# Performance work log

Hardware: AMD Instinct MI355X
Metric: run time of the kernel (lower is better)

The kernel has to match this reference:

```python
import jax, jax.numpy as jnp
import numpy as np

S, B, D = 2048, 2, 1024          # seq, batch, hidden
E, K = 64, 2                     # num_experts, top_k
I, SI = 512, 512                 # moe_intermediate, shared_expert_intermediate
CAP = 256                        # per-expert capacity; mean load = S*B*K/E = 128, 256 is >16 sigma -> no drops


def setup_inputs() -> dict:
    key = jax.random.key(0)
    ks = jax.random.split(key, 8)
    sc = lambda d: 1.0 / np.sqrt(d)
    return {
        "hidden_states": jax.random.normal(ks[0], (S, B, D), jnp.float32),
        "router_w": jax.random.normal(ks[1], (E, D), jnp.float32) * sc(D),          # FujiTopKRouter.weight
        "gate_up_proj": jax.random.normal(ks[2], (E, 2 * I, D), jnp.float32) * sc(D),
        "down_proj": jax.random.normal(ks[3], (E, D, I), jnp.float32) * sc(I),
        "sh_gate_w": jax.random.normal(ks[4], (SI, D), jnp.float32) * sc(D),
        "sh_up_w": jax.random.normal(ks[5], (SI, D), jnp.float32) * sc(D),
        "sh_down_w": jax.random.normal(ks[6], (D, SI), jnp.float32) * sc(SI),
        "sh_expert_gate_w": jax.random.normal(ks[7], (1, D), jnp.float32) * sc(D),
    }


def _moe(x, router_w, gate_up_proj, down_proj, sh_gate_w, sh_up_w, sh_down_w, sh_expert_gate_w):
    T = x.shape[0]
    # ---- shared expert (SwiGLU) + sigmoid gate ----
    shared = jnp.dot(jax.nn.silu(x @ sh_gate_w.T) * (x @ sh_up_w.T), sh_down_w.T)
    shared = jax.nn.sigmoid(x @ sh_expert_gate_w.T) * shared                      # [T, D]
    # ---- router: softmax (fp32) -> top-k -> normalize ----
    probs = jax.nn.softmax((x @ router_w.T).astype(jnp.float32), axis=-1)         # [T, E]
    top_w, top_i = jax.lax.top_k(probs, K)                                        # [T, K]
    top_w = top_w / (jnp.sum(top_w, axis=-1, keepdims=True) + 1e-9)
    top_w = top_w.astype(x.dtype)
    # ---- dispatch: permute (token, slot) pairs into fixed-capacity expert buffers ----
    e_f = top_i.reshape(-1)                                                       # [T*K] expert id per pair
    w_f = top_w.reshape(-1)                                                       # [T*K]
    tok = jnp.arange(T * K) // K                                                  # [T*K] source token
    oh = jax.nn.one_hot(e_f, E, dtype=jnp.int32)                                  # [T*K, E]
    pos = jnp.sum(jnp.cumsum(oh, axis=0) * oh, axis=-1) - 1                       # slot within expert
    buf = jnp.zeros((E, CAP, D), x.dtype).at[e_f, pos].set(x[tok])                # [E, C, D]
    # ---- per-expert SwiGLU as batched GEMMs ----
    h = jnp.einsum('ecd,eid->eci', buf, gate_up_proj)                             # [E, C, 2I]
    g, u = jnp.split(h, 2, axis=-1)
    y = jnp.einsum('eci,edi->ecd', jax.nn.silu(g) * u, down_proj)                 # [E, C, D]
    # ---- combine: gather back, weight, scatter-add to tokens ----
    routed = jnp.zeros_like(x).at[tok].add(y[e_f, pos] * w_f[:, None])            # [T, D]
    return shared + routed, probs


def reference(hidden_states, router_w, gate_up_proj, down_proj,
              sh_gate_w, sh_up_w, sh_down_w, sh_expert_gate_w):
    s, b, d = hidden_states.shape
    x = hidden_states.reshape(-1, d)
    out, router_logits = _moe(x, router_w, gate_up_proj, down_proj,
                              sh_gate_w, sh_up_w, sh_down_w, sh_expert_gate_w)
    return out.reshape(s, b, d), router_logits
```

## Files before the change

kernel.cpp:

```cpp
#include <hip/hip_runtime.h>
#include <hip/hip_bf16.h>
#include <stdint.h>

#define T_TOK 4096
#define DDIM  1024
#define NEXP  64
#define IDIM  512
#define SIDIM 512
#define CAP   256
#define LSTR  40

typedef __attribute__((ext_vector_type(4))) float f32x4;
typedef __attribute__((ext_vector_type(8))) short bf16x8;

__device__ __forceinline__ bf16x8 cvt8(f32x4 a, f32x4 b) {
    union { __hip_bfloat162 h[4]; bf16x8 v; } u;
    u.h[0] = __float22bfloat162_rn(make_float2(a[0], a[1]));
    u.h[1] = __float22bfloat162_rn(make_float2(a[2], a[3]));
    u.h[2] = __float22bfloat162_rn(make_float2(b[0], b[1]));
    u.h[3] = __float22bfloat162_rn(make_float2(b[2], b[3]));
    return u.v;
}
__device__ __forceinline__ short f2bs(float f) {
    union { __hip_bfloat16 h; short s; } u; u.h = __float2bfloat16(f); return u.s;
}

__global__ __launch_bounds__(256) void logits_kernel(const float* __restrict__ X,
                                                     const float* __restrict__ RW,
                                                     float* __restrict__ lpart) {
    __shared__ float sX[64 * 33];
    __shared__ float sW[64 * 33];
    int m0 = blockIdx.x * 64;
    int kz = blockIdx.y;
    int kbase = kz * 256;
    int tid = threadIdx.x;
    int tg = tid >> 4;
    int eg = tid & 15;
    float acc[4][4] = {};
    for (int k0 = 0; k0 < 256; k0 += 32) {
        __syncthreads();
#pragma unroll
        for (int i = 0; i < 8; ++i) {
            int idx = i * 256 + tid;
            int r = idx >> 5, c = idx & 31;
            sX[r * 33 + c] = X[(size_t)(m0 + r) * DDIM + kbase + k0 + c];
            sW[r * 33 + c] = RW[(size_t)r * DDIM + kbase + k0 + c];
        }
        __syncthreads();
#pragma unroll 4
        for (int k = 0; k < 32; ++k) {
            float xv[4], wv[4];
#pragma unroll
            for (int i = 0; i < 4; ++i) xv[i] = sX[(tg * 4 + i) * 33 + k];
#pragma unroll
            for (int j = 0; j < 4; ++j) wv[j] = sW[(eg * 4 + j) * 33 + k];
#pragma unroll
            for (int i = 0; i < 4; ++i)
#pragma unroll
                for (int j = 0; j < 4; ++j) acc[i][j] += xv[i] * wv[j];
        }
    }
    float* outp = lpart + (size_t)kz * T_TOK * NEXP;
#pragma unroll
    for (int i = 0; i < 4; ++i)
#pragma unroll
        for (int j = 0; j < 4; ++j)
            outp[(size_t)(m0 + tg * 4 + i) * NEXP + eg * 4 + j] = acc[i][j];
}

__global__ __launch_bounds__(256) void topk_kernel(const float* __restrict__ lpart,
                                                   const float* __restrict__ X,
                                                   const float* __restrict__ SEG,
                                                   float* __restrict__ probs_out,
                                                   int* __restrict__ counts,
                                                   int* __restrict__ tok_slot,
                                                   float* __restrict__ w_slot,
                                                   float* __restrict__ gate_sh) {
    int lane = threadIdx.x & 63;
    int wv   = threadIdx.x >> 6;
    int t    = blockIdx.x * 4 + wv;
    size_t li = (size_t)t * NEXP + lane;
    float l = lpart[li] + lpart[(size_t)T_TOK * NEXP + li]
            + lpart[2 * (size_t)T_TOK * NEXP + li] + lpart[3 * (size_t)T_TOK * NEXP + li];
    float mx = l;
    for (int s = 32; s; s >>= 1) mx = fmaxf(mx, __shfl_xor(mx, s));
    float e = __expf(l - mx);
    float sum = e;
    for (int s = 32; s; s >>= 1) sum += __shfl_xor(sum, s);
    float prob = e / sum;
    probs_out[li] = prob;
    float v = prob; int idx = lane;
    for (int s = 32; s; s >>= 1) {
        float ov = __shfl_xor(v, s); int oi = __shfl_xor(idx, s);
        if (ov > v || (ov == v && oi < idx)) { v = ov; idx = oi; }
    }
    float v1 = v; int i1 = idx;
    v = (lane == i1) ? -1e30f : prob; idx = lane;
    for (int s = 32; s; s >>= 1) {
        float ov = __shfl_xor(v, s); int oi = __shfl_xor(idx, s);
        if (ov > v || (ov == v && oi < idx)) { v = ov; idx = oi; }
    }
    float v2 = v; int i2 = idx;
    float denom = v1 + v2 + 1e-9f;
    if (lane == 0) {
        int s1 = atomicAdd(&counts[i1], 1);
        if (s1 < CAP) { tok_slot[i1 * CAP + s1] = t; w_slot[i1 * CAP + s1] = v1 / denom; }
        int s2 = atomicAdd(&counts[i2], 1);
        if (s2 < CAP) { tok_slot[i2 * CAP + s2] = t; w_slot[i2 * CAP + s2] = v2 / denom; }
    }
    float g = 0.f;
    const float* xr = X + (size_t)t * DDIM + lane * 16;
    const float* sr = SEG + lane * 16;
#pragma unroll
    for (int j = 0; j < 4; ++j) {
        f32x4 xv = *(const f32x4*)(xr + j * 4);
        f32x4 sv = *(const f32x4*)(sr + j * 4);
#pragma unroll
        for (int q = 0; q < 4; ++q) g += xv[q] * sv[q];
    }
    for (int s = 32; s; s >>= 1) g += __shfl_xor(g, s);
    if (lane == 0) gate_sh[t] = 1.f / (1.f + __expf(-g));
}

template <bool EXPERT>
__global__ __launch_bounds__(256) void gateup_kernel(const float* __restrict__ X,
                                                     const float* __restrict__ Wg_base,
                                                     const float* __restrict__ Wu_base,
                                                     const int* __restrict__ counts,
                                                     const int* __restrict__ tok_slot,
                                                     short* __restrict__ act_out) {
    __shared__ short sA[128 * LSTR];
    __shared__ short sBg[64 * LSTR];
    __shared__ short sBu[64 * LSTR];
    int e  = EXPERT ? blockIdx.z : 0;
    int m0 = blockIdx.y * 128;
    int n0 = blockIdx.x * 64;
    int M;
    const float *Wg, *Wu;
    if (EXPERT) {
        M = counts[e]; if (M > CAP) M = CAP;
        if (m0 >= M) return;
        const float* base = Wg_base + (size_t)e * (2 * IDIM) * DDIM;
        Wg = base; Wu = base + (size_t)IDIM * DDIM;
    } else {
        M = T_TOK; Wg = Wg_base; Wu = Wu_base;
    }
    int tid = threadIdx.x, lane = tid & 63, wv = tid >> 6;
    int wm = wv >> 1, wn = wv & 1;
    int srow = lane >> 2, scol8 = (lane & 3) * 8;
    const float* ag[2];
#pragma unroll
    for (int j = 0; j < 2; ++j) {
        int row = m0 + j * 64 + wv * 16 + srow;
        int grow;
        if (EXPERT) {
            int rr = (row < M) ? row : (M - 1);
            grow = tok_slot[e * CAP + rr];
        } else grow = row;
        ag[j] = X + (size_t)grow * DDIM + scol8;
    }
    const float* bgp = Wg + (size_t)(n0 + wv * 16 + srow) * DDIM + scol8;
    const float* bup = Wu + (size_t)(n0 + wv * 16 + srow) * DDIM + scol8;
    f32x4 accg[4][2] = {}; f32x4 accu[4][2] = {};
    int fm = lane & 15, fk = (lane >> 4) * 8;

    f32x4 r0[8], r1[8];
    auto loadt = [&](f32x4 (&r)[8], int k0) {
#pragma unroll
        for (int j = 0; j < 2; ++j) {
            r[j * 2 + 0] = *(const f32x4*)(ag[j] + k0);
            r[j * 2 + 1] = *(const f32x4*)(ag[j] + k0 + 4);
        }
        r[4] = *(const f32x4*)(bgp + k0); r[5] = *(const f32x4*)(bgp + k0 + 4);
        r[6] = *(const f32x4*)(bup + k0); r[7] = *(const f32x4*)(bup + k0 + 4);
    };
    auto stage = [&](const f32x4 (&r)[8]) {
        bf16x8 va0 = cvt8(r[0], r[1]);
        bf16x8 va1 = cvt8(r[2], r[3]);
        bf16x8 vg  = cvt8(r[4], r[5]);
        bf16x8 vu  = cvt8(r[6], r[7]);
        __syncthreads();
        *(bf16x8*)&sA[(wv * 16 + srow) * LSTR + scol8] = va0;
        *(bf16x8*)&sA[(64 + wv * 16 + srow) * LSTR + scol8] = va1;
        *(bf16x8*)&sBg[(wv * 16 + srow) * LSTR + scol8] = vg;
        *(bf16x8*)&sBu[(wv * 16 + srow) * LSTR + scol8] = vu;
        __syncthreads();
        bf16x8 bg[2], bu[2];
#pragma unroll
        for (int nt = 0; nt < 2; ++nt) {
            bg[nt] = *(const bf16x8*)&sBg[(wn * 32 + nt * 16 + fm) * LSTR + fk];
            bu[nt] = *(const bf16x8*)&sBu[(wn * 32 + nt * 16 + fm) * LSTR + fk];
        }
#pragma unroll
        for (int mt = 0; mt < 4; ++mt) {
            bf16x8 a = *(const bf16x8*)&sA[(wm * 64 + mt * 16 + fm) * LSTR + fk];
#pragma unroll
            for (int nt = 0; nt < 2; ++nt) {
                accg[mt][nt] = __builtin_amdgcn_mfma_f32_16x16x32_bf16(a, bg[nt], accg[mt][nt], 0, 0, 0);
                accu[mt][nt] = __builtin_amdgcn_mfma_f32_16x16x32_bf16(a, bu[nt], accu[mt][nt], 0, 0, 0);
            }
        }
    };
    loadt(r0, 0);
    for (int k0 = 0; k0 < DDIM; k0 += 64) {
        loadt(r1, k0 + 32);
        stage(r0);
        loadt(r0, (k0 + 64 < DDIM) ? (k0 + 64) : 0);
        stage(r1);
    }
    int frow = (lane >> 4) * 4, fcol = lane & 15;
    size_t out_base = EXPERT ? (size_t)e * CAP * IDIM : 0;
#pragma unroll
    for (int mt = 0; mt < 4; ++mt)
#pragma unroll
        for (int r = 0; r < 4; ++r) {
            int row = m0 + wm * 64 + mt * 16 + frow + r;
            if (row < M) {
#pragma unroll
                for (int nt = 0; nt < 2; ++nt) {
                    float g = accg[mt][nt][r];
                    float u = accu[mt][nt][r];
                    float a = (g / (1.f + __expf(-g))) * u;
                    act_out[out_base + (size_t)row * IDIM + (n0 + wn * 32 + nt * 16 + fcol)] = f2bs(a);
                }
            }
        }
}

template <bool EXPERT>
__global__ __launch_bounds__(256) void down_kernel(const short* __restrict__ A_base,
                                                   const float* __restrict__ W_base,
                                                   const int* __restrict__ counts,
                                                   const int* __restrict__ tok_slot,
                                                   const float* __restrict__ w_slot,
                                                   const float* __restrict__ gate_sh,
                                                   float* __restrict__ out) {
    __shared__ short sA[128 * LSTR];
    __shared__ short sB[128 * LSTR];
    const int KD = IDIM;
    int e  = EXPERT ? blockIdx.z : 0;
    int m0 = blockIdx.y * 128;
    int n0 = blockIdx.x * 128;
    int M;
    const short* A;
    const float* W;
    if (EXPERT) {
        M = counts[e]; if (M > CAP) M = CAP;
        if (m0 >= M) return;
        A = A_base + (size_t)e * CAP * IDIM;
        W = W_base + (size_t)e * DDIM * IDIM;
    } else { M = T_TOK; A = A_base; W = W_base; }
    int tid = threadIdx.x, lane = tid & 63, wv = tid >> 6;
    int wm = wv >> 1, wn = wv & 1;
    int srow = lane >> 2, scol8 = (lane & 3) * 8;
    const short* ap[2];
    const float* bp[2];
#pragma unroll
    for (int j = 0; j < 2; ++j) {
        int r = j * 64 + wv * 16 + srow;
        ap[j] = A + (size_t)(m0 + r) * KD + scol8;
        bp[j] = W + (size_t)(n0 + r) * KD + scol8;
    }
    f32x4 acc[4][4] = {};
    int fm = lane & 15, fk = (lane >> 4) * 8;

    struct Buf { bf16x8 a[2]; f32x4 b[4]; };
    Buf u0, u1;
    auto loadt = [&](Buf& r, int k0) {
#pragma unroll
        for (int j = 0; j < 2; ++j) {
            r.a[j] = *(const bf16x8*)(ap[j] + k0);
            r.b[j * 2 + 0] = *(const f32x4*)(bp[j] + k0);
            r.b[j * 2 + 1] = *(const f32x4*)(bp[j] + k0 + 4);
        }
    };
    auto stage = [&](const Buf& r) {
        bf16x8 vb0 = cvt8(r.b[0], r.b[1]);
        bf16x8 vb1 = cvt8(r.b[2], r.b[3]);
        __syncthreads();
        *(bf16x8*)&sA[(wv * 16 + srow) * LSTR + scol8] = r.a[0];
        *(bf16x8*)&sA[(64 + wv * 16 + srow) * LSTR + scol8] = r.a[1];
        *(bf16x8*)&sB[(wv * 16 + srow) * LSTR + scol8] = vb0;
        *(bf16x8*)&sB[(64 + wv * 16 + srow) * LSTR + scol8] = vb1;
        __syncthreads();
        bf16x8 b[4];
#pragma unroll
        for (int nt = 0; nt < 4; ++nt)
            b[nt] = *(const bf16x8*)&sB[(wn * 64 + nt * 16 + fm) * LSTR + fk];
#pragma unroll
        for (int mt = 0; mt < 4; ++mt) {
            bf16x8 a = *(const bf16x8*)&sA[(wm * 64 + mt * 16 + fm) * LSTR + fk];
#pragma unroll
            for (int nt = 0; nt < 4; ++nt)
                acc[mt][nt] = __builtin_amdgcn_mfma_f32_16x16x32_bf16(a, b[nt], acc[mt][nt], 0, 0, 0);
        }
    };
    loadt(u0, 0);
    for (int k0 = 0; k0 < KD; k0 += 64) {
        loadt(u1, k0 + 32);
        stage(u0);
        loadt(u0, (k0 + 64 < KD) ? (k0 + 64) : 0);
        stage(u1);
    }
    int frow = (lane >> 4) * 4, fcol = lane & 15;
#pragma unroll
    for (int mt = 0; mt < 4; ++mt)
#pragma unroll
        for (int r = 0; r < 4; ++r) {
            int row = m0 + wm * 64 + mt * 16 + frow + r;
            if (row >= M) continue;
            float scale; int trow;
            if (EXPERT) { scale = w_slot[e * CAP + row]; trow = tok_slot[e * CAP + row]; }
            else        { scale = gate_sh[row];          trow = row; }
#pragma unroll
            for (int nt = 0; nt < 4; ++nt) {
                int col = n0 + wn * 64 + nt * 16 + fcol;
                float vv = acc[mt][nt][r] * scale;
                if (EXPERT) atomicAdd(&out[(size_t)trow * DDIM + col], vv);
                else        out[(size_t)trow * DDIM + col] = vv;
            }
        }
}

extern "C" void kernel_launch(void* const* d_in, const int* in_sizes, int n_in,
                              void* d_out, int out_size, void* d_ws, size_t ws_size,
                              hipStream_t stream) {
    const float* X   = (const float*)d_in[0];
    const float* RW  = (const float*)d_in[1];
    const float* GUP = (const float*)d_in[2];
    const float* DW  = (const float*)d_in[3];
    const float* SG  = (const float*)d_in[4];
    const float* SU  = (const float*)d_in[5];
    const float* SD  = (const float*)d_in[6];
    const float* SEG = (const float*)d_in[7];
    float* out = (float*)d_out;

    char* ws = (char*)d_ws;
    size_t off = 0;
    float* lpart    = (float*)(ws + off); off += 4 * (size_t)T_TOK * NEXP * 4;
    int*   counts   = (int*)  (ws + off); off += 1024;
    int*   tok_slot = (int*)  (ws + off); off += (size_t)NEXP * CAP * 4;
    float* w_slot   = (float*)(ws + off); off += (size_t)NEXP * CAP * 4;
    float* gate_sh  = (float*)(ws + off); off += (size_t)T_TOK * 4;
    short* act      = (short*)(ws + off); off += (size_t)NEXP * CAP * IDIM * 2;
    short* act_sh   = (short*)(ws + off); off += (size_t)T_TOK * SIDIM * 2;
    (void)ws_size; (void)in_sizes; (void)n_in; (void)out_size;

    hipMemsetAsync(counts, 0, NEXP * sizeof(int), stream);
    logits_kernel<<<dim3(T_TOK / 64, 4), 256, 0, stream>>>(X, RW, lpart);
    topk_kernel<<<T_TOK / 4, 256, 0, stream>>>(lpart, X, SEG,
                                               out + (size_t)T_TOK * DDIM,
                                               counts, tok_slot, w_slot, gate_sh);
    gateup_kernel<false><<<dim3(SIDIM / 64, T_TOK / 128, 1), 256, 0, stream>>>(
        X, SG, SU, nullptr, nullptr, act_sh);
    gateup_kernel<true><<<dim3(IDIM / 64, CAP / 128, NEXP), 256, 0, stream>>>(
        X, GUP, GUP, counts, tok_slot, act);
    down_kernel<false><<<dim3(DDIM / 128, T_TOK / 128, 1), 256, 0, stream>>>(
        act_sh, SD, nullptr, nullptr, nullptr, gate_sh, out);
    down_kernel<true><<<dim3(DDIM / 128, CAP / 128, NEXP), 256, 0, stream>>>(
        act, DW, counts, tok_slot, w_slot, nullptr, out);
}
```

Before: 639.4 us.

## Stream GEMM tiles directly into swizzled LDS with async double buffering

The gate-up and down GEMM kernels stop staging tiles through registers with in-register bf16 conversion. They now issue global_load_lds copies of raw fp32 (and bf16 activation) tiles into XOR-swizzled, double-buffered LDS, and convert to bf16 when fragments are read. The goal is to overlap global loads with MFMA work and cut register pressure and VALU staging. In exchange, LDS use per block is larger, which is bounded by new occupancy hints, and the fp32-to-bf16 conversion is repeated by each wave that reads a fragment.

Measured after the change: 669.0 us. 4.6% more time.

```diff
diff --git a/kernel.cpp b/kernel.cpp
--- a/kernel.cpp
+++ b/kernel.cpp
@@ -8,7 +8,6 @@
 #define IDIM  512
 #define SIDIM 512
 #define CAP   256
-#define LSTR  40
 
 typedef __attribute__((ext_vector_type(4))) float f32x4;
 typedef __attribute__((ext_vector_type(8))) short bf16x8;
@@ -23,6 +22,19 @@
 }
 __device__ __forceinline__ short f2bs(float f) {
     union { __hip_bfloat16 h; short s; } u; u.h = __float2bfloat16(f); return u.s;
+}
+
+__device__ __forceinline__ void gload16(const void* g, void* l) {
+    __builtin_amdgcn_global_load_lds((const __attribute__((address_space(1))) void*)g,
+                                     (__attribute__((address_space(3))) void*)l, 16, 0, 0);
+}
+
+__device__ __forceinline__ bf16x8 frag32(const char* reg0, int row, int s) {
+    const char* p = reg0 + row * 128;
+    int sw = row & 7;
+    f32x4 lo = *(const f32x4*)(p + (((2 * s) ^ sw) << 4));
+    f32x4 hi = *(const f32x4*)(p + (((2 * s + 1) ^ sw) << 4));
+    return cvt8(lo, hi);
 }
 
 __global__ __launch_bounds__(256) void logits_kernel(const float* __restrict__ X,
@@ -123,15 +135,13 @@
 }
 
 template <bool EXPERT>
-__global__ __launch_bounds__(256) void gateup_kernel(const float* __restrict__ X,
-                                                     const float* __restrict__ Wg_base,
-                                                     const float* __restrict__ Wu_base,
-                                                     const int* __restrict__ counts,
-                                                     const int* __restrict__ tok_slot,
-                                                     short* __restrict__ act_out) {
-    __shared__ short sA[128 * LSTR];
-    __shared__ short sBg[64 * LSTR];
-    __shared__ short sBu[64 * LSTR];
+__global__ __launch_bounds__(256, 2) void gateup_kernel(const float* __restrict__ X,
+                                                        const float* __restrict__ Wg_base,
+                                                        const float* __restrict__ Wu_base,
+                                                        const int* __restrict__ counts,
+                                                        const int* __restrict__ tok_slot,
+                                                        short* __restrict__ act_out) {
+    __shared__ char smem[2 * 32768];
     int e  = EXPERT ? blockIdx.z : 0;
     int m0 = blockIdx.y * 128;
     int n0 = blockIdx.x * 64;
@@ -147,53 +157,51 @@
     }
     int tid = threadIdx.x, lane = tid & 63, wv = tid >> 6;
     int wm = wv >> 1, wn = wv & 1;
-    int srow = lane >> 2, scol8 = (lane & 3) * 8;
-    const float* ag[2];
-#pragma unroll
-    for (int j = 0; j < 2; ++j) {
-        int row = m0 + j * 64 + wv * 16 + srow;
+
+    int srow8 = tid >> 3;
+    int scol  = (tid & 7) ^ (srow8 & 7);
+    const float* gp[8];
+#pragma unroll
+    for (int t = 0; t < 4; ++t) {
+        int row = t * 32 + srow8;
         int grow;
         if (EXPERT) {
-            int rr = (row < M) ? row : (M - 1);
+            int rr = m0 + row; if (rr >= M) rr = M - 1;
             grow = tok_slot[e * CAP + rr];
-        } else grow = row;
-        ag[j] = X + (size_t)grow * DDIM + scol8;
-    }
-    const float* bgp = Wg + (size_t)(n0 + wv * 16 + srow) * DDIM + scol8;
-    const float* bup = Wu + (size_t)(n0 + wv * 16 + srow) * DDIM + scol8;
-    f32x4 accg[4][2] = {}; f32x4 accu[4][2] = {};
-    int fm = lane & 15, fk = (lane >> 4) * 8;
-
-    f32x4 r0[8], r1[8];
-    auto loadt = [&](f32x4 (&r)[8], int k0) {
-#pragma unroll
-        for (int j = 0; j < 2; ++j) {
-            r[j * 2 + 0] = *(const f32x4*)(ag[j] + k0);
-            r[j * 2 + 1] = *(const f32x4*)(ag[j] + k0 + 4);
-        }
-        r[4] = *(const f32x4*)(bgp + k0); r[5] = *(const f32x4*)(bgp + k0 + 4);
-        r[6] = *(const f32x4*)(bup + k0); r[7] = *(const f32x4*)(bup + k0 + 4);
+        } else grow = m0 + row;
+        gp[t] = X + (size_t)grow * DDIM + scol * 4;
+    }
+#pragma unroll
+    for (int t = 0; t < 2; ++t) {
+        int row = t * 32 + srow8;
+        gp[4 + t] = Wg + (size_t)(n0 + row) * DDIM + scol * 4;
+        gp[6 + t] = Wu + (size_t)(n0 + row) * DDIM + scol * 4;
+    }
+
+    auto issue = [&](int buf) {
+        char* lb = smem + buf * 32768 + wv * 1024;
+#pragma unroll
+        for (int t = 0; t < 8; ++t) {
+            gload16(gp[t], lb + t * 4096);
+            gp[t] += 32;
+        }
     };
-    auto stage = [&](const f32x4 (&r)[8]) {
-        bf16x8 va0 = cvt8(r[0], r[1]);
-        bf16x8 va1 = cvt8(r[2], r[3]);
-        bf16x8 vg  = cvt8(r[4], r[5]);
-        bf16x8 vu  = cvt8(r[6], r[7]);
-        __syncthreads();
-        *(bf16x8*)&sA[(wv * 16 + srow) * LSTR + scol8] = va0;
-        *(bf16x8*)&sA[(64 + wv * 16 + srow) * LSTR + scol8] = va1;
-        *(bf16x8*)&sBg[(wv * 16 + srow) * LSTR + scol8] = vg;
-        *(bf16x8*)&sBu[(wv * 16 + srow) * LSTR + scol8] = vu;
-        __syncthreads();
+
+    int fm = lane & 15, s = lane >> 4;
+    f32x4 accg[4][2] = {}, accu[4][2] = {};
+    auto compute = [&](int buf) {
+        const char* bb = smem + buf * 32768;
         bf16x8 bg[2], bu[2];
 #pragma unroll
         for (int nt = 0; nt < 2; ++nt) {
-            bg[nt] = *(const bf16x8*)&sBg[(wn * 32 + nt * 16 + fm) * LSTR + fk];
-            bu[nt] = *(const bf16x8*)&sBu[(wn * 32 + nt * 16 + fm) * LSTR + fk];
+            int row = wn * 32 + nt * 16 + fm;
+            bg[nt] = frag32(bb + 16384, row, s);
+            bu[nt] = frag32(bb + 24576, row, s);
         }
 #pragma unroll
         for (int mt = 0; mt < 4; ++mt) {
-            bf16x8 a = *(const bf16x8*)&sA[(wm * 64 + mt * 16 + fm) * LSTR + fk];
+            int row = wm * 64 + mt * 16 + fm;
+            bf16x8 a = frag32(bb, row, s);
 #pragma unroll
             for (int nt = 0; nt < 2; ++nt) {
                 accg[mt][nt] = __builtin_amdgcn_mfma_f32_16x16x32_bf16(a, bg[nt], accg[mt][nt], 0, 0, 0);
@@ -201,13 +209,18 @@
             }
         }
     };
-    loadt(r0, 0);
-    for (int k0 = 0; k0 < DDIM; k0 += 64) {
-        loadt(r1, k0 + 32);
-        stage(r0);
-        loadt(r0, (k0 + 64 < DDIM) ? (k0 + 64) : 0);
-        stage(r1);
-    }
+
+    issue(0);
+#pragma unroll 1
+    for (int kt = 0; kt < 32; kt += 2) {
+        __syncthreads();
+        issue(1);
+        compute(0);
+        __syncthreads();
+        if (kt + 2 < 32) issue(0);
+        compute(1);
+    }
+
     int frow = (lane >> 4) * 4, fcol = lane & 15;
     size_t out_base = EXPERT ? (size_t)e * CAP * IDIM : 0;
 #pragma unroll
@@ -228,15 +241,14 @@
 }
 
 template <bool EXPERT>
-__global__ __launch_bounds__(256) void down_kernel(const short* __restrict__ A_base,
-                                                   const float* __restrict__ W_base,
-                                                   const int* __restrict__ counts,
-                                                   const int* __restrict__ tok_slot,
-                                                   const float* __restrict__ w_slot,
-                                                   const float* __restrict__ gate_sh,
-                                                   float* __restrict__ out) {
-    __shared__ short sA[128 * LSTR];
-    __shared__ short sB[128 * LSTR];
+__global__ __launch_bounds__(256, 3) void down_kernel(const short* __restrict__ A_base,
+                                                      const float* __restrict__ W_base,
+                                                      const int* __restrict__ counts,
+                                                      const int* __restrict__ tok_slot,
+                                                      const float* __restrict__ w_slot,
+                                                      const float* __restrict__ gate_sh,
+                                                      float* __restrict__ out) {
+    __shared__ char smem[2 * 24576];
     const int KD = IDIM;
     int e  = EXPERT ? blockIdx.z : 0;
     int m0 = blockIdx.y * 128;
@@ -252,56 +264,70 @@
     } else { M = T_TOK; A = A_base; W = W_base; }
     int tid = threadIdx.x, lane = tid & 63, wv = tid >> 6;
     int wm = wv >> 1, wn = wv & 1;
-    int srow = lane >> 2, scol8 = (lane & 3) * 8;
+
     const short* ap[2];
-    const float* bp[2];
-#pragma unroll
-    for (int j = 0; j < 2; ++j) {
-        int r = j * 64 + wv * 16 + srow;
-        ap[j] = A + (size_t)(m0 + r) * KD + scol8;
-        bp[j] = W + (size_t)(n0 + r) * KD + scol8;
-    }
+#pragma unroll
+    for (int t = 0; t < 2; ++t) {
+        int row = t * 64 + (tid >> 2);
+        int col = (tid & 3) ^ ((tid >> 2) & 3);
+        ap[t] = A + (size_t)(m0 + row) * KD + col * 8;
+    }
+    const float* bp[4];
+    {
+        int srow8 = tid >> 3;
+        int col = (tid & 7) ^ (srow8 & 7);
+#pragma unroll
+        for (int t = 0; t < 4; ++t) {
+            int row = t * 32 + srow8;
+            bp[t] = W + (size_t)(n0 + row) * KD + col * 4;
+        }
+    }
+
+    auto issue = [&](int buf) {
+        char* lb = smem + buf * 24576 + wv * 1024;
+#pragma unroll
+        for (int t = 0; t < 2; ++t) {
+            gload16(ap[t], lb + t * 4096);
+            ap[t] += 32;
+        }
+#pragma unroll
+        for (int t = 0; t < 4; ++t) {
+            gload16(bp[t], lb + 8192 + t * 4096);
+            bp[t] += 32;
+        }
+    };
+
+    int fm = lane & 15, s = lane >> 4;
     f32x4 acc[4][4] = {};
-    int fm = lane & 15, fk = (lane >> 4) * 8;
-
-    struct Buf { bf16x8 a[2]; f32x4 b[4]; };
-    Buf u0, u1;
-    auto loadt = [&](Buf& r, int k0) {
-#pragma unroll
-        for (int j = 0; j < 2; ++j) {
-            r.a[j] = *(const bf16x8*)(ap[j] + k0);
-            r.b[j * 2 + 0] = *(const f32x4*)(bp[j] + k0);
-            r.b[j * 2 + 1] = *(const f32x4*)(bp[j] + k0 + 4);
-        }
-    };
-    auto stage = [&](const Buf& r) {
-        bf16x8 vb0 = cvt8(r.b[0], r.b[1]);
-        bf16x8 vb1 = cvt8(r.b[2], r.b[3]);
-        __syncthreads();
-        *(bf16x8*)&sA[(wv * 16 + srow) * LSTR + scol8] = r.a[0];
-        *(bf16x8*)&sA[(64 + wv * 16 + srow) * LSTR + scol8] = r.a[1];
-        *(bf16x8*)&sB[(wv * 16 + srow) * LSTR + scol8] = vb0;
-        *(bf16x8*)&sB[(64 + wv * 16 + srow) * LSTR + scol8] = vb1;
-        __syncthreads();
+    auto compute = [&](int buf) {
+        const char* bb = smem + buf * 24576;
         bf16x8 b[4];
 #pragma unroll
-        for (int nt = 0; nt < 4; ++nt)
-            b[nt] = *(const bf16x8*)&sB[(wn * 64 + nt * 16 + fm) * LSTR + fk];
+        for (int nt = 0; nt < 4; ++nt) {
+            int row = wn * 64 + nt * 16 + fm;
+            b[nt] = frag32(bb + 8192, row, s);
+        }
 #pragma unroll
         for (int mt = 0; mt < 4; ++mt) {
-            bf16x8 a = *(const bf16x8*)&sA[(wm * 64 + mt * 16 + fm) * LSTR + fk];
+            int row = wm * 64 + mt * 16 + fm;
+            bf16x8 a = *(const bf16x8*)(bb + row * 64 + ((s ^ (row & 3)) << 4));
 #pragma unroll
             for (int nt = 0; nt < 4; ++nt)
                 acc[mt][nt] = __builtin_amdgcn_mfma_f32_16x16x32_bf16(a, b[nt], acc[mt][nt], 0, 0, 0);
         }
     };
-    loadt(u0, 0);
-    for (int k0 = 0; k0 < KD; k0 += 64) {
-        loadt(u1, k0 + 32);
-        stage(u0);
-        loadt(u0, (k0 + 64 < KD) ? (k0 + 64) : 0);
-        stage(u1);
-    }
+
+    issue(0);
+#pragma unroll 1
+    for (int kt = 0; kt < 16; kt += 2) {
+        __syncthreads();
+        issue(1);
+        compute(0);
+        __syncthreads();
+        if (kt + 2 < 16) issue(0);
+        compute(1);
+    }
+
     int frow = (lane >> 4) * 4, fcol = lane & 15;
 #pragma unroll
     for (int mt = 0; mt < 4; ++mt)
```
